# Kernel tuning notes

Hardware: AMD Instinct MI355X
Metric: run time of the kernel (lower is better)

The kernel has to match this reference:

```python
import jax, jax.numpy as jnp
import numpy as np

KS = (3, 3)   # kernel_size
ST = (1, 1)   # stride
PD = (1, 1)   # padding
EPS = 1e-5


def unfold(x):
    """im2col matching torch.nn.Unfold: [B,C,H,W] -> [B, C*kh*kw, L] with (c,kh,kw) channel order, L row-major."""
    kh, kw = KS; sh, sw = ST; ph, pw = PD
    x = jnp.pad(x, ((0, 0), (0, 0), (ph, ph), (pw, pw)))
    B, C, H, W = x.shape
    Ho = (H - kh) // sh + 1
    Wo = (W - kw) // sw + 1
    I = (jnp.arange(Ho) * sh)[:, None, None, None] + jnp.arange(kh)[None, :, None, None]
    J = (jnp.arange(Wo) * sw)[None, None, :, None] + jnp.arange(kw)[None, None, None, :]
    p = x[:, :, I, J]  # [B, C, Ho, kh, Wo, kw]
    return p.transpose(0, 1, 3, 5, 2, 4).reshape(B, C * kh * kw, Ho * Wo)


def fold(cols, x_shape):
    """torch.nn.Fold is exactly the adjoint of Unfold (overlap-add)."""
    _, vjp = jax.vjp(unfold, jnp.zeros(x_shape, cols.dtype))
    return vjp(cols)[0]


def setup_inputs() -> dict:
    key = jax.random.key(0)
    k = jax.random.split(key, 6)
    B, C, H, W = 16, 64, 64, 64
    Cout, K = 64, KS[0] * KS[1]
    return {
        "x_mag": jax.random.uniform(k[0], (B, C, H, W), jnp.float32),
        "x_ang": jax.random.normal(k[1], (B, C, H, W), jnp.float32),
        "w_mag": jax.random.uniform(k[2], (C, K), jnp.float32),
        "w_ang": jax.random.uniform(k[3], (C, K), jnp.float32),
        "w1": jax.random.uniform(k[4], (C, K), jnp.float32),
        "w2": jax.random.uniform(k[5], (Cout, C), jnp.float32),
    }


def reference(x_mag, x_ang, w_mag, w_ang, w1, w2):
    B, C, H, W = x_mag.shape
    K = KS[0] * KS[1]
    Cout = w2.shape[0]
    Ho = (H + 2 * PD[0] - KS[0]) // ST[0] + 1
    Wo = (W + 2 * PD[1] - KS[1]) // ST[1] + 1

    # outer layer: unfold, mix with normalized weights, fold back (overlap-add)
    nws_mag = w_mag ** 2 / jnp.sum(w_mag ** 2)   # _normalize_weights_squared
    nw_ang = w_ang / jnp.sum(w_ang ** 2)         # _normalize_weights
    cm = unfold(x_mag).reshape(B, C, K, -1) + nws_mag[None, :, :, None]
    ca = unfold(x_ang).reshape(B, C, K, -1) * nw_ang[None, :, :, None]
    fm = fold(cm.reshape(B, C * K, -1), (B, C, H, W))
    fa = fold(ca.reshape(B, C * K, -1), (B, C, H, W))

    # helper: second unfold + weighted Frechet-mean reduction
    tbm = unfold(fm).reshape(B, C, K, -1)  # [B,C,K,L]
    tba = unfold(fa).reshape(B, C, K, -1)
    wmm1 = w1 ** 2 / jnp.sum(w1 ** 2, axis=1, keepdims=True)  # row-normalized
    wmm2 = w2 ** 2 / jnp.sum(w2 ** 2, axis=1, keepdims=True)
    wma1 = w1 ** 2 / jnp.sum(w1 ** 2)                          # globally normalized
    wma2 = w2 ** 2 / jnp.sum(w2 ** 2)

    m1 = jnp.einsum('bckl,ck->bcl', jnp.log(tbm + EPS), wmm1)
    out_mag = jnp.exp(jnp.einsum('bcl,oc->bol', m1, wmm2)).reshape(B, Cout, Ho, Wo)
    a1 = jnp.einsum('bckl,ck->bcl', tba, wma1)
    out_ang = jnp.einsum('bcl,oc->bol', a1, wma2).reshape(B, Cout, Ho, Wo)

    # from_polar -> stack (real, imag) on axis 1
    return jnp.stack([out_mag * jnp.cos(out_ang), out_mag * jnp.sin(out_ang)], axis=1)
```

## Files before the change

kernel.cpp:

```cpp
#include <hip/hip_runtime.h>
#include <math.h>

#define NB 16
#define NC 64
#define NL 4096
#define NCOUT 64
#define EPSF 1e-5f
#define LOG_EPSF -11.512925464970229f
#define CC 4
#define NCHUNK 16

#define FMA16(ACC, MV, W) \
  (ACC)[0].x = fmaf((MV).x,(W).x,(ACC)[0].x); (ACC)[0].y = fmaf((MV).y,(W).x,(ACC)[0].y); \
  (ACC)[0].z = fmaf((MV).z,(W).x,(ACC)[0].z); (ACC)[0].w = fmaf((MV).w,(W).x,(ACC)[0].w); \
  (ACC)[1].x = fmaf((MV).x,(W).y,(ACC)[1].x); (ACC)[1].y = fmaf((MV).y,(W).y,(ACC)[1].y); \
  (ACC)[1].z = fmaf((MV).z,(W).y,(ACC)[1].z); (ACC)[1].w = fmaf((MV).w,(W).y,(ACC)[1].w); \
  (ACC)[2].x = fmaf((MV).x,(W).z,(ACC)[2].x); (ACC)[2].y = fmaf((MV).y,(W).z,(ACC)[2].y); \
  (ACC)[2].z = fmaf((MV).z,(W).z,(ACC)[2].z); (ACC)[2].w = fmaf((MV).w,(W).z,(ACC)[2].w); \
  (ACC)[3].x = fmaf((MV).x,(W).w,(ACC)[3].x); (ACC)[3].y = fmaf((MV).y,(W).w,(ACC)[3].y); \
  (ACC)[3].z = fmaf((MV).z,(W).w,(ACC)[3].z); (ACC)[3].w = fmaf((MV).w,(W).w,(ACC)[3].w);

__global__ __launch_bounds__(256, 2) void fused_kernel(
    const float* __restrict__ x_mag, const float* __restrict__ x_ang,
    const float* __restrict__ wm, const float* __restrict__ wa,
    const float* __restrict__ w1, const float* __restrict__ w2,
    float* __restrict__ out)
{
    __shared__ __align__(16) float lfm[CC][4][72];
    __shared__ __align__(16) float fas[CC][4][72];
    __shared__ __align__(16) float m1r[2][CC][2][64];
    __shared__ __align__(16) float a1r[2][CC][2][64];
    __shared__ __align__(16) float w2m[64][68];
    __shared__ float smag_s[64][9], tang_s[64][9];
    __shared__ float red[4][4];
    __shared__ __align__(16) float rho[64];

    const int tid  = threadIdx.x;
    const int lane = tid & 63;
    const int wv   = tid >> 6;

    const int bid = (blockIdx.x & 7) * 64 + (blockIdx.x >> 3);
    const int b  = bid >> 5;
    const int i0 = (bid & 31) * 2;

    const int sr = lane >> 4;
    const int j4 = lane & 15;
    const int ir = i0 - 1 + sr;
    const bool ok = ((unsigned)ir < 64u);
    const int irc = ok ? ir : 0;
    const int ci = (ir == 0) ? 0 : ((ir == 63) ? 2 : 1);
    const int kL = ci * 3 + 0, kC = ci * 3 + 1, kR = ci * 3 + 2;
    const float ni = (ci == 1) ? 3.f : 2.f;
    const float nCt = 3.f * ni;
    const float n0 = (j4 == 0)  ? 2.f * ni : nCt;
    const float n3 = (j4 == 15) ? 2.f * ni : nCt;

    const float* spm = x_mag + ((size_t)(b * NC + wv) * NL + irc * 64 + j4 * 4);
    const float* spa = x_ang + ((size_t)(b * NC + wv) * NL + irc * 64 + j4 * 4);

    float4 pfm = *(const float4*)spm;
    float4 pfa = *(const float4*)spa;

    const int mrr = tid >> 7;
    const int o0  = ((tid >> 4) & 7) * 8;
    const int l0  = (tid & 15) * 4;

    float p0 = 0.f, p1 = 0.f, p2 = 0.f;
    {
        float v;
        v = wm[tid];       p0 += v * v;  v = wm[tid + 256]; p0 += v * v;
        v = wa[tid];       p1 += v * v;  v = wa[tid + 256]; p1 += v * v;
        v = w1[tid];       p2 += v * v;  v = w1[tid + 256]; p2 += v * v;
        if (tid < 64) {
            v = wm[tid + 512]; p0 += v * v;
            v = wa[tid + 512]; p1 += v * v;
            v = w1[tid + 512]; p2 += v * v;
        }
    }
    #pragma unroll
    for (int s = 32; s; s >>= 1) {
        p0 += __shfl_down(p0, s); p1 += __shfl_down(p1, s); p2 += __shfl_down(p2, s);
    }
    if (lane == 0) { red[0][wv] = p0; red[1][wv] = p1; red[2][wv] = p2; }

    float sqv[4][4], r2v[4][4];
    float s22p = 0.f;
    #pragma unroll
    for (int k = 0; k < 4; ++k) {
        const int oq = wv + 4 * k;
        #pragma unroll
        for (int n = 0; n < 4; ++n) {
            float v = w2[(oq * 4 + n) * 64 + lane];
            float s = v * v;
            sqv[k][n] = s;
            float rr_ = s;
            rr_ += __shfl_xor(rr_, 1);  rr_ += __shfl_xor(rr_, 2);
            rr_ += __shfl_xor(rr_, 4);  rr_ += __shfl_xor(rr_, 8);
            rr_ += __shfl_xor(rr_, 16); rr_ += __shfl_xor(rr_, 32);
            r2v[k][n] = rr_;
        }
        s22p += r2v[k][0] + r2v[k][1] + r2v[k][2] + r2v[k][3];
    }
    if (lane == 0) red[3][wv] = s22p;
    __syncthreads();
    const float s_wm2 = red[0][0] + red[0][1] + red[0][2] + red[0][3];
    const float s_wa2 = red[1][0] + red[1][1] + red[1][2] + red[1][3];
    const float s_w12 = red[2][0] + red[2][1] + red[2][2] + red[2][3];
    const float inv_s22 = 1.f / (red[3][0] + red[3][1] + red[3][2] + red[3][3]);
    const float inv_s12 = 1.f / s_w12;

    #pragma unroll
    for (int k = 0; k < 4; ++k) {
        const int oq = wv + 4 * k;
        float4 wmv4;
        wmv4.x = sqv[k][0] / r2v[k][0];
        wmv4.y = sqv[k][1] / r2v[k][1];
        wmv4.z = sqv[k][2] / r2v[k][2];
        wmv4.w = sqv[k][3] / r2v[k][3];
        *(float4*)&w2m[lane][oq * 4] = wmv4;
        if (lane == 0) {
            rho[oq * 4 + 0] = r2v[k][0] * inv_s22;
            rho[oq * 4 + 1] = r2v[k][1] * inv_s22;
            rho[oq * 4 + 2] = r2v[k][2] * inv_s22;
            rho[oq * 4 + 3] = r2v[k][3] * inv_s22;
        }
    }

    if (tid >= 64 && tid < 128) {
        const int c = tid - 64;
        float nm[9], na[9];
        const float inv_m = 1.f / s_wm2, inv_a = 1.f / s_wa2;
        #pragma unroll
        for (int k = 0; k < 9; ++k) {
            float v = wm[c * 9 + k];
            nm[k] = v * v * inv_m;
            na[k] = wa[c * 9 + k] * inv_a;
        }
        #pragma unroll
        for (int ci_ = 0; ci_ < 3; ++ci_) {
            #pragma unroll
            for (int cj = 0; cj < 3; ++cj) {
                float sm = 0.f, sa = 0.f;
                #pragma unroll
                for (int ki = 0; ki < 3; ++ki) {
                    bool vi = (ci_ == 0) ? (ki < 2) : ((ci_ == 2) ? (ki > 0) : true);
                    if (!vi) continue;
                    #pragma unroll
                    for (int kj = 0; kj < 3; ++kj) {
                        bool vj = (cj == 0) ? (kj < 2) : ((cj == 2) ? (kj > 0) : true);
                        if (!vj) continue;
                        sm += nm[ki * 3 + kj];
                        sa += na[ki * 3 + kj];
                    }
                }
                smag_s[c][ci_ * 3 + cj] = sm;
                tang_s[c][ci_ * 3 + cj] = sa;
            }
        }
    }

    if (j4 == 0)  { lfm[wv][sr][3]  = LOG_EPSF; fas[wv][sr][3]  = 0.f; }
    if (j4 == 15) { lfm[wv][sr][68] = LOG_EPSF; fas[wv][sr][68] = 0.f; }
    if (!ok) {
        float4 sm4; sm4.x = sm4.y = sm4.z = sm4.w = LOG_EPSF;
        float4 z4;  z4.x = z4.y = z4.z = z4.w = 0.f;
        *(float4*)&lfm[wv][sr][4 + j4 * 4] = sm4;
        *(float4*)&fas[wv][sr][4 + j4 * 4] = z4;
    }
    __syncthreads();

    float4 accm[8], acca[8];
    #pragma unroll
    for (int oi = 0; oi < 8; ++oi) {
        accm[oi].x = accm[oi].y = accm[oi].z = accm[oi].w = 0.f;
        acca[oi].x = acca[oi].y = acca[oi].z = acca[oi].w = 0.f;
    }

    auto do_matmul = [&](int chm, int pp) {
        const int c0 = chm * CC;
        #pragma unroll
        for (int cc = 0; cc < CC; ++cc) {
            float4 mv  = *(const float4*)&m1r[pp][cc][mrr][l0];
            float4 av  = *(const float4*)&a1r[pp][cc][mrr][l0];
            float4 w0_ = *(const float4*)&w2m[c0 + cc][o0];
            float4 w1_ = *(const float4*)&w2m[c0 + cc][o0 + 4];
            FMA16((&accm[0]), mv, w0_);
            FMA16((&accm[4]), mv, w1_);
            FMA16((&acca[0]), av, w0_);
            FMA16((&acca[4]), av, w1_);
        }
    };

    #pragma unroll 2
    for (int ch = 0; ch < NCHUNK; ++ch) {
        const int p = ch & 1;
        const int cg = ch * CC + wv;

        const int cgu = __builtin_amdgcn_readfirstlane(cg);
        const float* w1row = w1 + cgu * 9;
        float q[9];
        #pragma unroll
        for (int k = 0; k < 9; ++k) q[k] = w1row[k];

        if (ok) {
            float sC = smag_s[cg][kC], tC = tang_s[cg][kC];
            float s0 = (j4 == 0)  ? smag_s[cg][kL] : sC;
            float s3 = (j4 == 15) ? smag_s[cg][kR] : sC;
            float t0 = (j4 == 0)  ? tang_s[cg][kL] : tC;
            float t3 = (j4 == 15) ? tang_s[cg][kR] : tC;
            float4 dm, da;
            dm.x = __logf(fmaf(n0,  pfm.x, s0) + EPSF);
            dm.y = __logf(fmaf(nCt, pfm.y, sC) + EPSF);
            dm.z = __logf(fmaf(nCt, pfm.z, sC) + EPSF);
            dm.w = __logf(fmaf(n3,  pfm.w, s3) + EPSF);
            da.x = pfa.x * t0; da.y = pfa.y * tC;
            da.z = pfa.z * tC; da.w = pfa.w * t3;
            *(float4*)&lfm[wv][sr][4 + j4 * 4] = dm;
            *(float4*)&fas[wv][sr][4 + j4 * 4] = da;
        }

        if (ch + 1 < NCHUNK) {
            pfm = *(const float4*)(spm + (size_t)(ch + 1) * CC * NL);
            pfa = *(const float4*)(spa + (size_t)(ch + 1) * CC * NL);
        }

        if (ch > 0) do_matmul(ch - 1, p ^ 1);

        #pragma unroll
        for (int k = 0; k < 9; ++k) q[k] = q[k] * q[k];
        const float r1c = ((q[0] + q[1]) + (q[2] + q[3])) + ((q[4] + q[5]) + (q[6] + q[7])) + q[8];
        const float inv_r1 = 1.f / r1c;

        {
            float mres0 = 0.f, mres1 = 0.f, ares0 = 0.f, ares1 = 0.f;
            #pragma unroll
            for (int r_ = 0; r_ < 4; ++r_) {
                float l0v = lfm[wv][r_][lane + 3];
                float l1v = lfm[wv][r_][lane + 4];
                float l2v = lfm[wv][r_][lane + 5];
                float a0v = fas[wv][r_][lane + 3];
                float a1v = fas[wv][r_][lane + 4];
                float a2v = fas[wv][r_][lane + 5];
                if (r_ < 3) {
                    mres0 = fmaf(q[r_ * 3 + 0], l0v, mres0);
                    mres0 = fmaf(q[r_ * 3 + 1], l1v, mres0);
                    mres0 = fmaf(q[r_ * 3 + 2], l2v, mres0);
                    ares0 = fmaf(q[r_ * 3 + 0], a0v, ares0);
                    ares0 = fmaf(q[r_ * 3 + 1], a1v, ares0);
                    ares0 = fmaf(q[r_ * 3 + 2], a2v, ares0);
                }
                if (r_ > 0) {
                    const int ki = r_ - 1;
                    mres1 = fmaf(q[ki * 3 + 0], l0v, mres1);
                    mres1 = fmaf(q[ki * 3 + 1], l1v, mres1);
                    mres1 = fmaf(q[ki * 3 + 2], l2v, mres1);
                    ares1 = fmaf(q[ki * 3 + 0], a0v, ares1);
                    ares1 = fmaf(q[ki * 3 + 1], a1v, ares1);
                    ares1 = fmaf(q[ki * 3 + 2], a2v, ares1);
                }
            }
            m1r[p][wv][0][lane] = mres0 * inv_r1;
            m1r[p][wv][1][lane] = mres1 * inv_r1;
            a1r[p][wv][0][lane] = ares0 * inv_s12;
            a1r[p][wv][1][lane] = ares1 * inv_s12;
        }
        __syncthreads();
    }
    do_matmul(NCHUNK - 1, 1);

    {
        const float4 rh0 = *(const float4*)&rho[o0];
        const float4 rh1 = *(const float4*)&rho[o0 + 4];
        acca[0].x *= rh0.x; acca[0].y *= rh0.x; acca[0].z *= rh0.x; acca[0].w *= rh0.x;
        acca[1].x *= rh0.y; acca[1].y *= rh0.y; acca[1].z *= rh0.y; acca[1].w *= rh0.y;
        acca[2].x *= rh0.z; acca[2].y *= rh0.z; acca[2].z *= rh0.z; acca[2].w *= rh0.z;
        acca[3].x *= rh0.w; acca[3].y *= rh0.w; acca[3].z *= rh0.w; acca[3].w *= rh0.w;
        acca[4].x *= rh1.x; acca[4].y *= rh1.x; acca[4].z *= rh1.x; acca[4].w *= rh1.x;
        acca[5].x *= rh1.y; acca[5].y *= rh1.y; acca[5].z *= rh1.y; acca[5].w *= rh1.y;
        acca[6].x *= rh1.z; acca[6].y *= rh1.z; acca[6].z *= rh1.z; acca[6].w *= rh1.z;
        acca[7].x *= rh1.w; acca[7].y *= rh1.w; acca[7].z *= rh1.w; acca[7].w *= rh1.w;
    }

    #pragma unroll
    for (int oi = 0; oi < 8; ++oi) {
        float4 am = accm[oi], aa = acca[oi];
        float4 oc, os;
        float ex;
        ex = __expf(am.x); oc.x = ex * __cosf(aa.x); os.x = ex * __sinf(aa.x);
        ex = __expf(am.y); oc.y = ex * __cosf(aa.y); os.y = ex * __sinf(aa.y);
        ex = __expf(am.z); oc.z = ex * __cosf(aa.z); os.z = ex * __sinf(aa.z);
        ex = __expf(am.w); oc.w = ex * __cosf(aa.w); os.w = ex * __sinf(aa.w);
        size_t gi = ((size_t)(b * 2) * NCOUT + o0 + oi) * NL + (size_t)(i0 + mrr) * 64 + l0;
        *(float4*)&out[gi] = oc;
        *(float4*)&out[gi + (size_t)NCOUT * NL] = os;
    }
}

extern "C" void kernel_launch(void* const* d_in, const int* in_sizes, int n_in,
                              void* d_out, int out_size, void* d_ws, size_t ws_size,
                              hipStream_t stream) {
    const float* x_mag = (const float*)d_in[0];
    const float* x_ang = (const float*)d_in[1];
    const float* w_mag = (const float*)d_in[2];
    const float* w_ang = (const float*)d_in[3];
    const float* w1    = (const float*)d_in[4];
    const float* w2    = (const float*)d_in[5];
    float* out = (float*)d_out;

    fused_kernel<<<NB * 32, 256, 0, stream>>>(x_mag, x_ang, w_mag, w_ang, w1, w2, out);
}
```

Measured before the change: 39.97 us.

## Hoist weight normalization into a prep kernel and interleave mag/ang in LDS

Moves the per-block weight reductions, w2 row normalization, rho and boundary-sum tables into a separate small prep kernel that writes them to workspace. The main kernel then reads these from global memory (w2 transposed weights now come from global/L2 inside the matmul instead of LDS). Magnitude and angle rows are interleaved in one LDS buffer so the 3x3 reduction uses packed 2-wide FMAs. This removes redundant setup work repeated by all 512 blocks and shrinks LDS use, at the cost of an extra launch and global loads in the inner matmul.

```diff
diff --git a/kernel.cpp b/kernel.cpp
--- a/kernel.cpp
+++ b/kernel.cpp
@@ -4,11 +4,18 @@
 #define NB 16
 #define NC 64
 #define NL 4096
-#define NCOUT 64
 #define EPSF 1e-5f
 #define LOG_EPSF -11.512925464970229f
 #define CC 4
 #define NCHUNK 16
+
+#define WS_W2T   0
+#define WS_RHO   4096
+#define WS_SMAG  4160
+#define WS_TANG  4736
+#define WS_IS12  5312
+
+typedef float f32x2 __attribute__((ext_vector_type(2)));
 
 #define FMA16(ACC, MV, W) \
   (ACC)[0].x = fmaf((MV).x,(W).x,(ACC)[0].x); (ACC)[0].y = fmaf((MV).y,(W).x,(ACC)[0].y); \
@@ -20,20 +27,102 @@
   (ACC)[3].x = fmaf((MV).x,(W).w,(ACC)[3].x); (ACC)[3].y = fmaf((MV).y,(W).w,(ACC)[3].y); \
   (ACC)[3].z = fmaf((MV).z,(W).w,(ACC)[3].z); (ACC)[3].w = fmaf((MV).w,(W).w,(ACC)[3].w);
 
+__global__ __launch_bounds__(256) void prep_kernel(
+    const float* __restrict__ wm, const float* __restrict__ wa,
+    const float* __restrict__ w1, const float* __restrict__ w2,
+    float* __restrict__ ws)
+{
+    __shared__ float r2s[64];
+    __shared__ float red[3][4];
+    const int tid  = threadIdx.x;
+    const int lane = tid & 63;
+    const int wv   = tid >> 6;
+
+    if (tid < 64) {
+        float s = 0.f;
+        for (int c = 0; c < 64; ++c) { float v = w2[tid * 64 + c]; s = fmaf(v, v, s); }
+        r2s[tid] = s;
+    }
+    float p0 = 0.f, p1 = 0.f, p2 = 0.f;
+    {
+        float v;
+        v = wm[tid]; p0 += v * v;  v = wm[tid + 256]; p0 += v * v;
+        v = wa[tid]; p1 += v * v;  v = wa[tid + 256]; p1 += v * v;
+        v = w1[tid]; p2 += v * v;  v = w1[tid + 256]; p2 += v * v;
+        if (tid < 64) {
+            v = wm[tid + 512]; p0 += v * v;
+            v = wa[tid + 512]; p1 += v * v;
+            v = w1[tid + 512]; p2 += v * v;
+        }
+    }
+    #pragma unroll
+    for (int s = 32; s; s >>= 1) {
+        p0 += __shfl_down(p0, s); p1 += __shfl_down(p1, s); p2 += __shfl_down(p2, s);
+    }
+    if (lane == 0) { red[0][wv] = p0; red[1][wv] = p1; red[2][wv] = p2; }
+    __syncthreads();
+    const float s_wm2 = red[0][0] + red[0][1] + red[0][2] + red[0][3];
+    const float s_wa2 = red[1][0] + red[1][1] + red[1][2] + red[1][3];
+    const float s_w12 = red[2][0] + red[2][1] + red[2][2] + red[2][3];
+
+    const int c0 = blockIdx.x * 4;
+    {
+        int c = c0 + (tid >> 6), o = tid & 63;
+        float v = w2[o * 64 + c];
+        ws[WS_W2T + c * 64 + o] = v * v / r2s[o];
+    }
+
+    if (blockIdx.x == 0) {
+        if (tid < 64) {
+            float s22 = 0.f;
+            #pragma unroll
+            for (int o = 0; o < 64; ++o) s22 += r2s[o];
+            ws[WS_RHO + tid] = r2s[tid] / s22;
+
+            const int c = tid;
+            float nm[9], na[9];
+            const float inv_m = 1.f / s_wm2, inv_a = 1.f / s_wa2;
+            #pragma unroll
+            for (int k = 0; k < 9; ++k) {
+                float v = wm[c * 9 + k];
+                nm[k] = v * v * inv_m;
+                na[k] = wa[c * 9 + k] * inv_a;
+            }
+            #pragma unroll
+            for (int ci_ = 0; ci_ < 3; ++ci_) {
+                #pragma unroll
+                for (int cj = 0; cj < 3; ++cj) {
+                    float sm = 0.f, sa = 0.f;
+                    #pragma unroll
+                    for (int ki = 0; ki < 3; ++ki) {
+                        bool vi = (ci_ == 0) ? (ki < 2) : ((ci_ == 2) ? (ki > 0) : true);
+                        if (!vi) continue;
+                        #pragma unroll
+                        for (int kj = 0; kj < 3; ++kj) {
+                            bool vj = (cj == 0) ? (kj < 2) : ((cj == 2) ? (kj > 0) : true);
+                            if (!vj) continue;
+                            sm += nm[ki * 3 + kj];
+                            sa += na[ki * 3 + kj];
+                        }
+                    }
+                    ws[WS_SMAG + c * 9 + ci_ * 3 + cj] = sm;
+                    ws[WS_TANG + c * 9 + ci_ * 3 + cj] = sa;
+                }
+            }
+        }
+        if (tid == 0) ws[WS_IS12] = 1.f / s_w12;
+    }
+}
+
 __global__ __launch_bounds__(256, 2) void fused_kernel(
     const float* __restrict__ x_mag, const float* __restrict__ x_ang,
-    const float* __restrict__ wm, const float* __restrict__ wa,
-    const float* __restrict__ w1, const float* __restrict__ w2,
+    const float* __restrict__ w1, const float* __restrict__ ws,
     float* __restrict__ out)
 {
-    __shared__ __align__(16) float lfm[CC][4][72];
-    __shared__ __align__(16) float fas[CC][4][72];
+    __shared__ __align__(16) float lf2[CC][4][144];
     __shared__ __align__(16) float m1r[2][CC][2][64];
     __shared__ __align__(16) float a1r[2][CC][2][64];
-    __shared__ __align__(16) float w2m[64][68];
-    __shared__ float smag_s[64][9], tang_s[64][9];
-    __shared__ float red[4][4];
-    __shared__ __align__(16) float rho[64];
+    __shared__ float smag_s[576], tang_s[576];
 
     const int tid  = threadIdx.x;
     const int lane = tid & 63;
@@ -65,107 +154,31 @@
     const int o0  = ((tid >> 4) & 7) * 8;
     const int l0  = (tid & 15) * 4;
 
-    float p0 = 0.f, p1 = 0.f, p2 = 0.f;
+    const float* w2t_g = ws + WS_W2T;
+    const float inv_s12 = ws[WS_IS12];
+
     {
-        float v;
-        v = wm[tid];       p0 += v * v;  v = wm[tid + 256]; p0 += v * v;
-        v = wa[tid];       p1 += v * v;  v = wa[tid + 256]; p1 += v * v;
-        v = w1[tid];       p2 += v * v;  v = w1[tid + 256]; p2 += v * v;
-        if (tid < 64) {
-            v = wm[tid + 512]; p0 += v * v;
-            v = wa[tid + 512]; p1 += v * v;
-            v = w1[tid + 512]; p2 += v * v;
-        }
-    }
-    #pragma unroll
-    for (int s = 32; s; s >>= 1) {
-        p0 += __shfl_down(p0, s); p1 += __shfl_down(p1, s); p2 += __shfl_down(p2, s);
-    }
-    if (lane == 0) { red[0][wv] = p0; red[1][wv] = p1; red[2][wv] = p2; }
-
-    float sqv[4][4], r2v[4][4];
-    float s22p = 0.f;
-    #pragma unroll
-    for (int k = 0; k < 4; ++k) {
-        const int oq = wv + 4 * k;
-        #pragma unroll
-        for (int n = 0; n < 4; ++n) {
-            float v = w2[(oq * 4 + n) * 64 + lane];
-            float s = v * v;
-            sqv[k][n] = s;
-            float rr_ = s;
-            rr_ += __shfl_xor(rr_, 1);  rr_ += __shfl_xor(rr_, 2);
-            rr_ += __shfl_xor(rr_, 4);  rr_ += __shfl_xor(rr_, 8);
-            rr_ += __shfl_xor(rr_, 16); rr_ += __shfl_xor(rr_, 32);
-            r2v[k][n] = rr_;
-        }
-        s22p += r2v[k][0] + r2v[k][1] + r2v[k][2] + r2v[k][3];
-    }
-    if (lane == 0) red[3][wv] = s22p;
-    __syncthreads();
-    const float s_wm2 = red[0][0] + red[0][1] + red[0][2] + red[0][3];
-    const float s_wa2 = red[1][0] + red[1][1] + red[1][2] + red[1][3];
-    const float s_w12 = red[2][0] + red[2][1] + red[2][2] + red[2][3];
-    const float inv_s22 = 1.f / (red[3][0] + red[3][1] + red[3][2] + red[3][3]);
-    const float inv_s12 = 1.f / s_w12;
-
-    #pragma unroll
-    for (int k = 0; k < 4; ++k) {
-        const int oq = wv + 4 * k;
-        float4 wmv4;
-        wmv4.x = sqv[k][0] / r2v[k][0];
-        wmv4.y = sqv[k][1] / r2v[k][1];
-        wmv4.z = sqv[k][2] / r2v[k][2];
-        wmv4.w = sqv[k][3] / r2v[k][3];
-        *(float4*)&w2m[lane][oq * 4] = wmv4;
-        if (lane == 0) {
-            rho[oq * 4 + 0] = r2v[k][0] * inv_s22;
-            rho[oq * 4 + 1] = r2v[k][1] * inv_s22;
-            rho[oq * 4 + 2] = r2v[k][2] * inv_s22;
-            rho[oq * 4 + 3] = r2v[k][3] * inv_s22;
-        }
-    }
-
-    if (tid >= 64 && tid < 128) {
-        const int c = tid - 64;
-        float nm[9], na[9];
-        const float inv_m = 1.f / s_wm2, inv_a = 1.f / s_wa2;
-        #pragma unroll
-        for (int k = 0; k < 9; ++k) {
-            float v = wm[c * 9 + k];
-            nm[k] = v * v * inv_m;
-            na[k] = wa[c * 9 + k] * inv_a;
-        }
-        #pragma unroll
-        for (int ci_ = 0; ci_ < 3; ++ci_) {
-            #pragma unroll
-            for (int cj = 0; cj < 3; ++cj) {
-                float sm = 0.f, sa = 0.f;
-                #pragma unroll
-                for (int ki = 0; ki < 3; ++ki) {
-                    bool vi = (ci_ == 0) ? (ki < 2) : ((ci_ == 2) ? (ki > 0) : true);
-                    if (!vi) continue;
-                    #pragma unroll
-                    for (int kj = 0; kj < 3; ++kj) {
-                        bool vj = (cj == 0) ? (kj < 2) : ((cj == 2) ? (kj > 0) : true);
-                        if (!vj) continue;
-                        sm += nm[ki * 3 + kj];
-                        sa += na[ki * 3 + kj];
-                    }
-                }
-                smag_s[c][ci_ * 3 + cj] = sm;
-                tang_s[c][ci_ * 3 + cj] = sa;
-            }
-        }
-    }
-
-    if (j4 == 0)  { lfm[wv][sr][3]  = LOG_EPSF; fas[wv][sr][3]  = 0.f; }
-    if (j4 == 15) { lfm[wv][sr][68] = LOG_EPSF; fas[wv][sr][68] = 0.f; }
+        float4 v0 = ((const float4*)(ws + WS_SMAG))[tid & 127];
+        if (tid < 128) *(float4*)&smag_s[tid * 4] = v0;
+        else           *(float4*)&tang_s[(tid - 128) * 4] = v0;
+        if (tid < 16)  smag_s[512 + tid * 4 + 0] = ws[WS_SMAG + 512 + tid * 4 + 0],
+                       smag_s[512 + tid * 4 + 1] = ws[WS_SMAG + 512 + tid * 4 + 1],
+                       smag_s[512 + tid * 4 + 2] = ws[WS_SMAG + 512 + tid * 4 + 2],
+                       smag_s[512 + tid * 4 + 3] = ws[WS_SMAG + 512 + tid * 4 + 3];
+        else if (tid < 32) {
+            int t = tid - 16;
+            tang_s[512 + t * 4 + 0] = ws[WS_TANG + 512 + t * 4 + 0];
+            tang_s[512 + t * 4 + 1] = ws[WS_TANG + 512 + t * 4 + 1];
+            tang_s[512 + t * 4 + 2] = ws[WS_TANG + 512 + t * 4 + 2];
+            tang_s[512 + t * 4 + 3] = ws[WS_TANG + 512 + t * 4 + 3];
+        }
+    }
+    if (j4 == 0)  { lf2[wv][sr][6]   = LOG_EPSF; lf2[wv][sr][7]   = 0.f; }
+    if (j4 == 15) { lf2[wv][sr][136] = LOG_EPSF; lf2[wv][sr][137] = 0.f; }
     if (!ok) {
-        float4 sm4; sm4.x = sm4.y = sm4.z = sm4.w = LOG_EPSF;
-        float4 z4;  z4.x = z4.y = z4.z = z4.w = 0.f;
-        *(float4*)&lfm[wv][sr][4 + j4 * 4] = sm4;
-        *(float4*)&fas[wv][sr][4 + j4 * 4] = z4;
+        float4 s4; s4.x = LOG_EPSF; s4.y = 0.f; s4.z = LOG_EPSF; s4.w = 0.f;
+        *(float4*)&lf2[wv][sr][8 + 8 * j4]  = s4;
+        *(float4*)&lf2[wv][sr][12 + 8 * j4] = s4;
     }
     __syncthreads();
 
@@ -180,10 +193,11 @@
         const int c0 = chm * CC;
         #pragma unroll
         for (int cc = 0; cc < CC; ++cc) {
+            const float* wg = w2t_g + (size_t)(c0 + cc) * 64 + o0;
+            float4 w0_ = *(const float4*)(wg);
+            float4 w1_ = *(const float4*)(wg + 4);
             float4 mv  = *(const float4*)&m1r[pp][cc][mrr][l0];
             float4 av  = *(const float4*)&a1r[pp][cc][mrr][l0];
-            float4 w0_ = *(const float4*)&w2m[c0 + cc][o0];
-            float4 w1_ = *(const float4*)&w2m[c0 + cc][o0 + 4];
             FMA16((&accm[0]), mv, w0_);
             FMA16((&accm[4]), mv, w1_);
             FMA16((&acca[0]), av, w0_);
@@ -203,20 +217,22 @@
         for (int k = 0; k < 9; ++k) q[k] = w1row[k];
 
         if (ok) {
-            float sC = smag_s[cg][kC], tC = tang_s[cg][kC];
-            float s0 = (j4 == 0)  ? smag_s[cg][kL] : sC;
-            float s3 = (j4 == 15) ? smag_s[cg][kR] : sC;
-            float t0 = (j4 == 0)  ? tang_s[cg][kL] : tC;
-            float t3 = (j4 == 15) ? tang_s[cg][kR] : tC;
-            float4 dm, da;
-            dm.x = __logf(fmaf(n0,  pfm.x, s0) + EPSF);
-            dm.y = __logf(fmaf(nCt, pfm.y, sC) + EPSF);
-            dm.z = __logf(fmaf(nCt, pfm.z, sC) + EPSF);
-            dm.w = __logf(fmaf(n3,  pfm.w, s3) + EPSF);
-            da.x = pfa.x * t0; da.y = pfa.y * tC;
-            da.z = pfa.z * tC; da.w = pfa.w * t3;
-            *(float4*)&lfm[wv][sr][4 + j4 * 4] = dm;
-            *(float4*)&fas[wv][sr][4 + j4 * 4] = da;
+            float sC = smag_s[cg * 9 + kC], tC = tang_s[cg * 9 + kC];
+            float s0 = (j4 == 0)  ? smag_s[cg * 9 + kL] : sC;
+            float s3 = (j4 == 15) ? smag_s[cg * 9 + kR] : sC;
+            float t0 = (j4 == 0)  ? tang_s[cg * 9 + kL] : tC;
+            float t3 = (j4 == 15) ? tang_s[cg * 9 + kR] : tC;
+            float4 v0, v1;
+            v0.x = __logf(fmaf(n0,  pfm.x, s0) + EPSF);
+            v0.y = pfa.x * t0;
+            v0.z = __logf(fmaf(nCt, pfm.y, sC) + EPSF);
+            v0.w = pfa.y * tC;
+            v1.x = __logf(fmaf(nCt, pfm.z, sC) + EPSF);
+            v1.y = pfa.z * tC;
+            v1.z = __logf(fmaf(n3,  pfm.w, s3) + EPSF);
+            v1.w = pfa.w * t3;
+            *(float4*)&lf2[wv][sr][8 + 8 * j4]  = v0;
+            *(float4*)&lf2[wv][sr][12 + 8 * j4] = v1;
         }
 
         if (ch + 1 < NCHUNK) {
@@ -230,47 +246,43 @@
         for (int k = 0; k < 9; ++k) q[k] = q[k] * q[k];
         const float r1c = ((q[0] + q[1]) + (q[2] + q[3])) + ((q[4] + q[5]) + (q[6] + q[7])) + q[8];
         const float inv_r1 = 1.f / r1c;
+        f32x2 q2[9];
+        #pragma unroll
+        for (int k = 0; k < 9; ++k) { q2[k].x = q[k]; q2[k].y = q[k]; }
 
         {
-            float mres0 = 0.f, mres1 = 0.f, ares0 = 0.f, ares1 = 0.f;
+            f32x2 a0; a0.x = 0.f; a0.y = 0.f;
+            f32x2 a1; a1.x = 0.f; a1.y = 0.f;
             #pragma unroll
             for (int r_ = 0; r_ < 4; ++r_) {
-                float l0v = lfm[wv][r_][lane + 3];
-                float l1v = lfm[wv][r_][lane + 4];
-                float l2v = lfm[wv][r_][lane + 5];
-                float a0v = fas[wv][r_][lane + 3];
-                float a1v = fas[wv][r_][lane + 4];
-                float a2v = fas[wv][r_][lane + 5];
+                const float* rp = &lf2[wv][r_][0];
+                f32x2 v0 = *(const f32x2*)(rp + 2 * lane + 6);
+                f32x2 v1 = *(const f32x2*)(rp + 2 * lane + 8);
+                f32x2 v2 = *(const f32x2*)(rp + 2 * lane + 10);
                 if (r_ < 3) {
-                    mres0 = fmaf(q[r_ * 3 + 0], l0v, mres0);
-                    mres0 = fmaf(q[r_ * 3 + 1], l1v, mres0);
-                    mres0 = fmaf(q[r_ * 3 + 2], l2v, mres0);
-                    ares0 = fmaf(q[r_ * 3 + 0], a0v, ares0);
-                    ares0 = fmaf(q[r_ * 3 + 1], a1v, ares0);
-                    ares0 = fmaf(q[r_ * 3 + 2], a2v, ares0);
+                    a0 = __builtin_elementwise_fma(q2[r_ * 3 + 0], v0, a0);
+                    a0 = __builtin_elementwise_fma(q2[r_ * 3 + 1], v1, a0);
+                    a0 = __builtin_elementwise_fma(q2[r_ * 3 + 2], v2, a0);
                 }
                 if (r_ > 0) {
                     const int ki = r_ - 1;
-                    mres1 = fmaf(q[ki * 3 + 0], l0v, mres1);
-                    mres1 = fmaf(q[ki * 3 + 1], l1v, mres1);
-                    mres1 = fmaf(q[ki * 3 + 2], l2v, mres1);
-                    ares1 = fmaf(q[ki * 3 + 0], a0v, ares1);
-                    ares1 = fmaf(q[ki * 3 + 1], a1v, ares1);
-                    ares1 = fmaf(q[ki * 3 + 2], a2v, ares1);
+                    a1 = __builtin_elementwise_fma(q2[ki * 3 + 0], v0, a1);
+                    a1 = __builtin_elementwise_fma(q2[ki * 3 + 1], v1, a1);
+                    a1 = __builtin_elementwise_fma(q2[ki * 3 + 2], v2, a1);
                 }
             }
-            m1r[p][wv][0][lane] = mres0 * inv_r1;
-            m1r[p][wv][1][lane] = mres1 * inv_r1;
-            a1r[p][wv][0][lane] = ares0 * inv_s12;
-            a1r[p][wv][1][lane] = ares1 * inv_s12;
+            m1r[p][wv][0][lane] = a0.x * inv_r1;
+            a1r[p][wv][0][lane] = a0.y * inv_s12;
+            m1r[p][wv][1][lane] = a1.x * inv_r1;
+            a1r[p][wv][1][lane] = a1.y * inv_s12;
         }
         __syncthreads();
     }
     do_matmul(NCHUNK - 1, 1);
 
     {
-        const float4 rh0 = *(const float4*)&rho[o0];
-        const float4 rh1 = *(const float4*)&rho[o0 + 4];
+        const float4 rh0 = *(const float4*)(ws + WS_RHO + o0);
+        const float4 rh1 = *(const float4*)(ws + WS_RHO + o0 + 4);
         acca[0].x *= rh0.x; acca[0].y *= rh0.x; acca[0].z *= rh0.x; acca[0].w *= rh0.x;
         acca[1].x *= rh0.y; acca[1].y *= rh0.y; acca[1].z *= rh0.y; acca[1].w *= rh0.y;
         acca[2].x *= rh0.z; acca[2].y *= rh0.z; acca[2].z *= rh0.z; acca[2].w *= rh0.z;
@@ -290,9 +302,9 @@
         ex = __expf(am.y); oc.y = ex * __cosf(aa.y); os.y = ex * __sinf(aa.y);
         ex = __expf(am.z); oc.z = ex * __cosf(aa.z); os.z = ex * __sinf(aa.z);
         ex = __expf(am.w); oc.w = ex * __cosf(aa.w); os.w = ex * __sinf(aa.w);
-        size_t gi = ((size_t)(b * 2) * NCOUT + o0 + oi) * NL + (size_t)(i0 + mrr) * 64 + l0;
+        size_t gi = ((size_t)(b * 2) * NC + o0 + oi) * NL + (size_t)(i0 + mrr) * 64 + l0;
         *(float4*)&out[gi] = oc;
-        *(float4*)&out[gi + (size_t)NCOUT * NL] = os;
+        *(float4*)&out[gi + (size_t)NC * NL] = os;
     }
 }
 
@@ -306,6 +318,8 @@
     const float* w1    = (const float*)d_in[4];
     const float* w2    = (const float*)d_in[5];
     float* out = (float*)d_out;
-
-    fused_kernel<<<NB * 32, 256, 0, stream>>>(x_mag, x_ang, w_mag, w_ang, w1, w2, out);
+    float* ws  = (float*)d_ws;
+
+    prep_kernel<<<16, 256, 0, stream>>>(w_mag, w_ang, w1, w2, ws);
+    fused_kernel<<<NB * 32, 256, 0, stream>>>(x_mag, x_ang, w1, ws, out);
 }
```

Measured after the change: 41.22 us. 1.03x slower.
